# Performance work log

Hardware: AMD Instinct MI355X
Metric: run time of the kernel (lower is better)

Reference implementation:

```python
import jax, jax.numpy as jnp
import numpy as np

TEMP = 0.07  # init temperature
EPS = 1e-12  # F.normalize eps


def _per_cloud_loss(fmap, labels):
    # fmap: [C, N] per-point features; labels: [N] int
    v = fmap.T  # [N, C]
    v = v / jnp.maximum(jnp.linalg.norm(v, axis=1, keepdims=True), EPS)
    # NxN similarity, exp then divide by temp (order matches original)
    dot = jnp.exp(v @ v.T) / TEMP  # [N, N]
    dot = dot - jnp.diag(jnp.diag(dot))  # zero the diagonal
    mask = (labels[:, None] == labels[None, :]).astype(dot.dtype)  # [N, N]
    mask_not = 1.0 - mask
    pos = (mask * dot).sum(1) / mask.sum(1)  # note: denom includes self, as in original
    neg = (mask_not * dot).sum(1) / mask_not.sum(1)
    return jnp.mean(-jnp.log(pos / (pos + neg)))


def setup_inputs() -> dict:
    key = jax.random.key(0)
    k1, k2 = jax.random.split(key)
    B, C, N = 8, 128, 4096
    features = jax.random.normal(k1, (B, C, N), dtype=jnp.float32)
    labels_all = jax.random.randint(k2, (B, N), 0, 16, dtype=jnp.int64)
    return {"features": features, "labels_all": labels_all}


def reference(features, labels_all):
    losses = jax.vmap(_per_cloud_loss)(features, labels_all)  # [B]
    return jnp.mean(losses)
```

## Files before the change

kernel.cpp:

```cpp
#include <hip/hip_runtime.h>
#include <stdint.h>

#define NPTS 4096
#define NC 128
#define NB 8
#define CSPLIT 8
#define COLS_PER (NPTS / CSPLIT)
#define RPB 128

typedef __bf16 bf16x8 __attribute__((ext_vector_type(8)));
typedef float f32x4 __attribute__((ext_vector_type(4)));
typedef unsigned short u16;
typedef unsigned int u32;

__device__ inline float fast_exp2(float x) { return __builtin_amdgcn_exp2f(x); }

__device__ inline u16 f2bf(float x) {
    u32 u = __float_as_uint(x);
    u32 r = (u + 0x7fffu + ((u >> 16) & 1u)) >> 16;
    return (u16)r;
}

__global__ __launch_bounds__(256) void norm_count_kernel(const float* __restrict__ feat,
                                                         const int* __restrict__ labels,
                                                         u16* __restrict__ vbf,
                                                         int* __restrict__ counts,
                                                         u32* __restrict__ zbase) {
    int b = blockIdx.y;
    int tid = threadIdx.x;
    if (blockIdx.x == 64) {
        if (b == 0 && tid < 2) zbase[tid] = 0u;
        __shared__ int h[16];
        if (tid < 16) h[tid] = 0;
        __syncthreads();
        for (int n = tid; n < NPTS; n += 256)
            atomicAdd(&h[labels[b * NPTS + n] & 15], 1);
        __syncthreads();
        if (tid < 16) counts[b * 16 + tid] = h[tid];
        return;
    }
    int n0 = blockIdx.x * 64;
    __shared__ float tile[64][129];
    __shared__ float part[8][64];
    __shared__ float rn[64];
    const float* fb = feat + (size_t)b * NC * NPTS;
    int nslot = tid & 31;
    int ty = tid >> 5;
    float s0 = 0.f, s1 = 0.f;
#pragma unroll
    for (int i = 0; i < 16; ++i) {
        int c = i * 8 + ty;
        float2 x = *(const float2*)(fb + (size_t)c * NPTS + n0 + 2 * nslot);
        tile[2 * nslot][c] = x.x;
        tile[2 * nslot + 1][c] = x.y;
        s0 += x.x * x.x;
        s1 += x.y * x.y;
    }
    part[ty][2 * nslot] = s0;
    part[ty][2 * nslot + 1] = s1;
    __syncthreads();
    if (tid < 64) {
        float s = 0.f;
#pragma unroll
        for (int t = 0; t < 8; ++t) s += part[t][tid];
        rn[tid] = 1.f / fmaxf(sqrtf(s), 1e-12f);
    }
    __syncthreads();
    u32* out = (u32*)vbf;
    size_t obase = ((size_t)b * NPTS + n0) * (NC / 2);
#pragma unroll
    for (int i = 0; i < 16; ++i) {
        int idx = tid + i * 256;
        int p = idx >> 6, k = idx & 63;
        float r = rn[p];
        float x0 = tile[p][2 * k] * r;
        float x1 = tile[p][2 * k + 1] * r;
        out[obase + (size_t)p * 64 + k] = (u32)f2bf(x0) | ((u32)f2bf(x1) << 16);
    }
}

__global__ __launch_bounds__(256, 2) void sim_kernel(const u16* __restrict__ vbf,
                                                     const int* __restrict__ labels,
                                                     float2* __restrict__ rowacc) {
    int bid = blockIdx.x;
    int rt = bid >> 6;
    int combo = bid & 63;
    int b = combo >> 3;
    int cs = combo & 7;
    int row0 = rt * RPB;
    int c0 = cs * COLS_PER;
    int tid = threadIdx.x;
    int wave = tid >> 6, lane = tid & 63;
    int quad = lane >> 4, ln = lane & 15;

    const u16* vb = vbf + (size_t)b * NPTS * NC;
    const int* lab = labels + b * NPTS;

    int rbase[2];
    rbase[0] = row0 + wave * 32;
    rbase[1] = rbase[0] + 16;

    bf16x8 afrag[2][4];
#pragma unroll
    for (int s = 0; s < 2; ++s)
#pragma unroll
        for (int f = 0; f < 4; ++f) {
            bf16x8 v = *(const bf16x8*)(vb + (size_t)(rbase[s] + ln) * NC + f * 32 + quad * 8);
#pragma unroll
            for (int k = 0; k < 8; ++k) v[k] = (__bf16)((float)v[k] * 1.44269504f);
            afrag[s][f] = v;
        }

    int lrow[2][4];
#pragma unroll
    for (int s = 0; s < 2; ++s)
#pragma unroll
        for (int r = 0; r < 4; ++r) lrow[s][r] = lab[rbase[s] + quad * 4 + r];

    int diagct[2], diagsub[2];
#pragma unroll
    for (int s = 0; s < 2; ++s) {
        diagct[s] = rbase[s] & ~63;
        diagsub[s] = (rbase[s] >> 4) & 3;
    }

    float psame[2][4] = {{0.f}}, sall[2][4] = {{0.f}};

    __shared__ u16 cols[64 * 128];
    __shared__ int clab[64];

    const uint4* src = (const uint4*)(vb + (size_t)c0 * NC);
    u32 woff[4];
#pragma unroll
    for (int i = 0; i < 4; ++i) {
        int idx = tid + i * 256;
        int rr = idx >> 4, cc = idx & 15;
        woff[i] = rr * 128 + ((cc ^ (rr & 15)) * 8);
    }

    for (int t = 0; t < COLS_PER / 64; ++t) {
        int ct = c0 + t * 64;
        __syncthreads();
#pragma unroll
        for (int i = 0; i < 4; ++i)
            *(uint4*)(cols + woff[i]) = src[t * 1024 + tid + i * 256];
        if (tid < 64) clab[tid] = lab[ct + tid];
        __syncthreads();

#pragma unroll
        for (int sub = 0; sub < 4; ++sub) {
            const u16* rowb = cols + (sub * 16 + ln) * 128;
            bf16x8 bfrag[4];
#pragma unroll
            for (int f = 0; f < 4; ++f)
                bfrag[f] = *(const bf16x8*)(rowb + (((4 * f + quad) ^ ln) * 8));
            int lc = clab[sub * 16 + ln];
#pragma unroll
            for (int s = 0; s < 2; ++s) {
                f32x4 d = {0.f, 0.f, 0.f, 0.f};
#pragma unroll
                for (int f = 0; f < 4; ++f)
                    d = __builtin_amdgcn_mfma_f32_16x16x32_bf16(afrag[s][f], bfrag[f], d, 0, 0, 0);
                if (ct == diagct[s] && sub == diagsub[s]) {
#pragma unroll
                    for (int r = 0; r < 4; ++r) {
                        float e = fast_exp2(d[r]);
                        if (ln == quad * 4 + r) e = 0.f;
                        sall[s][r] += e;
                        psame[s][r] += (lc == lrow[s][r]) ? e : 0.f;
                    }
                } else {
#pragma unroll
                    for (int r = 0; r < 4; ++r) {
                        float e = fast_exp2(d[r]);
                        sall[s][r] += e;
                        psame[s][r] += (lc == lrow[s][r]) ? e : 0.f;
                    }
                }
            }
        }
    }

#pragma unroll
    for (int off = 1; off < 16; off <<= 1)
#pragma unroll
        for (int s = 0; s < 2; ++s)
#pragma unroll
            for (int r = 0; r < 4; ++r) {
                psame[s][r] += __shfl_xor(psame[s][r], off);
                sall[s][r] += __shfl_xor(sall[s][r], off);
            }
    if (ln == 0) {
#pragma unroll
        for (int s = 0; s < 2; ++s)
#pragma unroll
            for (int r = 0; r < 4; ++r)
                rowacc[((size_t)cs * NB + b) * NPTS + rbase[s] + quad * 4 + r] =
                    make_float2(psame[s][r], sall[s][r]);
    }
}

__global__ __launch_bounds__(256) void loss_kernel(const float2* __restrict__ rowacc,
                                                   const int* __restrict__ labels,
                                                   const int* __restrict__ counts,
                                                   float* __restrict__ acc,
                                                   u32* __restrict__ ticket,
                                                   float* __restrict__ out) {
    int idx = blockIdx.x * 256 + threadIdx.x;
    int b = idx >> 12;
    float ps = 0.f, sa = 0.f;
#pragma unroll
    for (int cs = 0; cs < CSPLIT; ++cs) {
        float2 v = rowacc[(size_t)cs * NB * NPTS + idx];
        ps += v.x;
        sa += v.y;
    }
    int lb = labels[idx] & 15;
    int cnt = counts[b * 16 + lb];
    float p = ps / (float)cnt;
    float n = (sa - ps) / (float)(NPTS - cnt);
    float loss = -__logf(p / (p + n));
#pragma unroll
    for (int off = 1; off < 64; off <<= 1) loss += __shfl_xor(loss, off);
    __shared__ float w[4];
    if ((threadIdx.x & 63) == 0) w[threadIdx.x >> 6] = loss;
    __syncthreads();
    if (threadIdx.x == 0) {
        atomicAdd(acc, w[0] + w[1] + w[2] + w[3]);
        __threadfence();
        u32 t = atomicAdd(ticket, 1u);
        if (t == gridDim.x - 1) {
            float v = atomicAdd(acc, 0.f);
            out[0] = v * (1.f / (float)(NB * NPTS));
        }
    }
}

extern "C" void kernel_launch(void* const* d_in, const int* in_sizes, int n_in,
                              void* d_out, int out_size, void* d_ws, size_t ws_size,
                              hipStream_t stream) {
    const float* feat = (const float*)d_in[0];
    const int* labels = (const int*)d_in[1];
    float* out = (float*)d_out;

    float* acc = (float*)d_ws;
    u32* ticket = (u32*)((char*)d_ws + 4);
    int* counts = (int*)((char*)d_ws + 256);
    float2* rowacc = (float2*)((char*)d_ws + 4096);
    u16* vbf = (u16*)((char*)d_ws + 4096 + (size_t)CSPLIT * NB * NPTS * 8);

    norm_count_kernel<<<dim3(65, NB), 256, 0, stream>>>(feat, labels, vbf, counts, (u32*)d_ws);
    sim_kernel<<<dim3(32 * 64), 256, 0, stream>>>(vbf, labels, rowacc);
    loss_kernel<<<dim3(NB * NPTS / 256), 256, 0, stream>>>(rowacc, labels, counts, acc, ticket, out);
}
```

Before: 132.0 us.

## Double-buffer column tiles in LDS with register prefetch in sim_kernel

The sim kernel now keeps two shared-memory column tiles. The next tile's global loads go into registers before the MFMA/exp work on the current tile and are stored to the other buffer afterwards. This overlaps global load latency with compute and cuts the barriers per tile from two to one. In exchange LDS use doubles to about 33KB per block and register pressure rises from the prefetch registers, which could affect occupancy at 2 blocks per CU.

```diff
diff --git a/kernel.cpp b/kernel.cpp
--- a/kernel.cpp
+++ b/kernel.cpp
@@ -78,6 +78,39 @@
         out[obase + (size_t)p * 64 + k] = (u32)f2bf(x0) | ((u32)f2bf(x1) << 16);
     }
 }
+
+#define COMPUTE_TILE(BUFI, CT)                                                  \
+    {                                                                           \
+        int ct_ = (CT);                                                         \
+        _Pragma("unroll") for (int sub = 0; sub < 4; ++sub) {                   \
+            const u16* rowb = cols[BUFI] + (sub * 16 + ln) * 128;               \
+            bf16x8 bfrag[4];                                                    \
+            _Pragma("unroll") for (int f = 0; f < 4; ++f)                       \
+                bfrag[f] = *(const bf16x8*)(rowb + (((4 * f + quad) ^ ln) * 8));\
+            int lc = clab[BUFI][sub * 16 + ln];                                 \
+            _Pragma("unroll") for (int s = 0; s < 2; ++s) {                     \
+                f32x4 d = {0.f, 0.f, 0.f, 0.f};                                 \
+                _Pragma("unroll") for (int f = 0; f < 4; ++f)                   \
+                    d = __builtin_amdgcn_mfma_f32_16x16x32_bf16(afrag[s][f],    \
+                                                                bfrag[f], d,    \
+                                                                0, 0, 0);       \
+                if (ct_ == diagct[s] && sub == diagsub[s]) {                    \
+                    _Pragma("unroll") for (int r = 0; r < 4; ++r) {             \
+                        float e = fast_exp2(d[r]);                              \
+                        if (ln == quad * 4 + r) e = 0.f;                        \
+                        sall[s][r] += e;                                        \
+                        psame[s][r] += (lc == lrow[s][r]) ? e : 0.f;            \
+                    }                                                           \
+                } else {                                                        \
+                    _Pragma("unroll") for (int r = 0; r < 4; ++r) {             \
+                        float e = fast_exp2(d[r]);                              \
+                        sall[s][r] += e;                                        \
+                        psame[s][r] += (lc == lrow[s][r]) ? e : 0.f;            \
+                    }                                                           \
+                }                                                               \
+            }                                                                   \
+        }                                                                       \
+    }
 
 __global__ __launch_bounds__(256, 2) void sim_kernel(const u16* __restrict__ vbf,
                                                      const int* __restrict__ labels,
@@ -126,8 +159,8 @@
 
     float psame[2][4] = {{0.f}}, sall[2][4] = {{0.f}};
 
-    __shared__ u16 cols[64 * 128];
-    __shared__ int clab[64];
+    __shared__ u16 cols[2][64 * 128];
+    __shared__ int clab[2][64];
 
     const uint4* src = (const uint4*)(vb + (size_t)c0 * NC);
     u32 woff[4];
@@ -138,47 +171,46 @@
         woff[i] = rr * 128 + ((cc ^ (rr & 15)) * 8);
     }
 
-    for (int t = 0; t < COLS_PER / 64; ++t) {
-        int ct = c0 + t * 64;
-        __syncthreads();
-#pragma unroll
-        for (int i = 0; i < 4; ++i)
-            *(uint4*)(cols + woff[i]) = src[t * 1024 + tid + i * 256];
-        if (tid < 64) clab[tid] = lab[ct + tid];
-        __syncthreads();
-
-#pragma unroll
-        for (int sub = 0; sub < 4; ++sub) {
-            const u16* rowb = cols + (sub * 16 + ln) * 128;
-            bf16x8 bfrag[4];
-#pragma unroll
-            for (int f = 0; f < 4; ++f)
-                bfrag[f] = *(const bf16x8*)(rowb + (((4 * f + quad) ^ ln) * 8));
-            int lc = clab[sub * 16 + ln];
-#pragma unroll
-            for (int s = 0; s < 2; ++s) {
-                f32x4 d = {0.f, 0.f, 0.f, 0.f};
-#pragma unroll
-                for (int f = 0; f < 4; ++f)
-                    d = __builtin_amdgcn_mfma_f32_16x16x32_bf16(afrag[s][f], bfrag[f], d, 0, 0, 0);
-                if (ct == diagct[s] && sub == diagsub[s]) {
-#pragma unroll
-                    for (int r = 0; r < 4; ++r) {
-                        float e = fast_exp2(d[r]);
-                        if (ln == quad * 4 + r) e = 0.f;
-                        sall[s][r] += e;
-                        psame[s][r] += (lc == lrow[s][r]) ? e : 0.f;
-                    }
-                } else {
-#pragma unroll
-                    for (int r = 0; r < 4; ++r) {
-                        float e = fast_exp2(d[r]);
-                        sall[s][r] += e;
-                        psame[s][r] += (lc == lrow[s][r]) ? e : 0.f;
-                    }
-                }
+    {
+        uint4 pf[4];
+#pragma unroll
+        for (int i = 0; i < 4; ++i) pf[i] = src[tid + i * 256];
+        int pl = (tid < 64) ? lab[c0 + tid] : 0;
+#pragma unroll
+        for (int i = 0; i < 4; ++i) *(uint4*)(cols[0] + woff[i]) = pf[i];
+        if (tid < 64) clab[0][tid] = pl;
+    }
+    __syncthreads();
+
+    for (int tp = 0; tp < 4; ++tp) {
+        int t0 = 2 * tp;
+        {
+            uint4 pf[4];
+#pragma unroll
+            for (int i = 0; i < 4; ++i) pf[i] = src[(t0 + 1) * 1024 + tid + i * 256];
+            int pl = (tid < 64) ? lab[c0 + (t0 + 1) * 64 + tid] : 0;
+            COMPUTE_TILE(0, c0 + t0 * 64);
+#pragma unroll
+            for (int i = 0; i < 4; ++i) *(uint4*)(cols[1] + woff[i]) = pf[i];
+            if (tid < 64) clab[1][tid] = pl;
+        }
+        __syncthreads();
+        {
+            uint4 pf[4];
+            int pl = 0;
+            if (tp < 3) {
+#pragma unroll
+                for (int i = 0; i < 4; ++i) pf[i] = src[(t0 + 2) * 1024 + tid + i * 256];
+                pl = (tid < 64) ? lab[c0 + (t0 + 2) * 64 + tid] : 0;
             }
-        }
+            COMPUTE_TILE(1, c0 + (t0 + 1) * 64);
+            if (tp < 3) {
+#pragma unroll
+                for (int i = 0; i < 4; ++i) *(uint4*)(cols[0] + woff[i]) = pf[i];
+                if (tid < 64) clab[0][tid] = pl;
+            }
+        }
+        __syncthreads();
     }
 
 #pragma unroll
```

After: 154.7 us. +17.2%, slower.
